# Performance work log

Hardware: AMD Instinct MI355X
Metric: run time of the kernel (lower is better)

Reference implementation:

```python
import jax, jax.numpy as jnp
import numpy as np

G, NPG, MAXN = 1024, 40, 51   # graphs, nodes/graph, dense pad size
EPG = 80                       # edges per graph
N, E = G * NPG, G * EPG
D_IN, D_OUT, D_EDGE = 64, 32, 16


def _lin(key, fan_in, shape):
    b = 1.0 / np.sqrt(fan_in)
    return jax.random.uniform(key, shape, jnp.float32, -b, b)


def setup_inputs() -> dict:
    key = jax.random.key(0)
    ks = jax.random.split(key, 24)
    node_features = jax.random.randint(ks[0], (N, 9), 0, 128)
    edge_features = jax.random.randint(ks[1], (E, 3), 0, 8)
    offs = jnp.repeat(jnp.arange(G) * NPG, EPG)
    src = jax.random.randint(ks[2], (E,), 0, NPG) + offs
    dst = jax.random.randint(ks[3], (E,), 0, NPG) + offs
    edge_index = jnp.stack([src, dst])
    batch = jnp.repeat(jnp.arange(G), NPG)
    inp = dict(node_features=node_features, edge_features=edge_features,
               edge_index=edge_index, batch=batch)
    # OGB-style encoders: one embedding table per feature column, summed
    inp['atom_emb'] = jax.random.normal(ks[4], (9, 128, D_IN), jnp.float32) * 0.1
    inp['bond_emb'] = jax.random.normal(ks[5], (3, 8, D_EDGE), jnp.float32) * 0.1
    # edge-conditioned weight MLP: 16 -> 1024 -> 256 -> 64*32 (no bias)
    inp['gW1'] = _lin(ks[6], 16, (16, 1024))
    inp['gW2'] = _lin(ks[7], 1024, (1024, 256))
    inp['gW3'] = _lin(ks[8], 256, (256, D_IN * D_OUT))
    # NNConv root weight + bias
    inp['root'] = _lin(ks[9], D_IN, (D_IN, D_OUT))
    inp['conv_bias'] = jnp.zeros((D_OUT,), jnp.float32)
    # readout MLP: 51*32 -> 256 -> 128 -> 32 -> 8 -> 1
    dims = [MAXN * D_OUT, 256, 128, 32, 8, 1]
    for i in range(5):
        inp[f'mW{i+1}'] = _lin(ks[10 + 2 * i], dims[i], (dims[i], dims[i + 1]))
        inp[f'mb{i+1}'] = _lin(ks[11 + 2 * i], dims[i], (dims[i + 1],))
    return inp


def reference(node_features, edge_features, edge_index, batch,
              atom_emb, bond_emb, gW1, gW2, gW3, root, conv_bias,
              mW1, mb1, mW2, mb2, mW3, mb3, mW4, mb4, mW5, mb5):
    # encoders: sum of per-column embeddings
    x = jnp.sum(atom_emb[jnp.arange(9), node_features], axis=1)      # [N,64]
    e = jnp.sum(bond_emb[jnp.arange(3), edge_features], axis=1)      # [E,16]
    # per-edge weight matrix via MLP
    h = jax.nn.relu(e @ gW1)
    h = jax.nn.relu(h @ gW2)
    w = (h @ gW3).reshape(-1, D_IN, D_OUT)                           # [E,64,32]
    # NNConv: gather src, per-edge matmul, scatter-add to dst, + root + bias
    src, dst = edge_index[0], edge_index[1]
    msg = jnp.einsum('ed,edo->eo', x[src], w)                        # [E,32]
    agg = jax.ops.segment_sum(msg, dst, num_segments=N)              # [N,32]
    out = agg + x @ root + conv_bias
    # to_dense_batch(max_num_nodes=51); exactly NPG nodes per graph, zero-pad
    dense = jnp.zeros((G, MAXN, D_OUT), out.dtype).at[:, :NPG].set(
        out.reshape(G, NPG, D_OUT))
    f = dense.reshape(G, MAXN * D_OUT)                               # [G,1632]
    f = jax.nn.relu(f @ mW1 + mb1)
    f = jax.nn.relu(f @ mW2 + mb2)
    f = jax.nn.relu(f @ mW3 + mb3)
    f = jax.nn.relu(f @ mW4 + mb4)
    return f @ mW5 + mb5                                             # [G,1]
```

## Files before the change

### kernel.cpp

```cpp
#include <hip/hip_runtime.h>

#define NNODES 40960
#define NEDGES 81920
#define NG     1024
#define NCOMBO 512
#define NHB    320
#define NGRP   4

__global__ __launch_bounds__(256) void k_node(
    const int* __restrict__ nf, const float* __restrict__ emb,
    const float* __restrict__ root, const float* __restrict__ bias,
    float* __restrict__ x, float* __restrict__ out) {
    __shared__ float sx[4][64];
    const int t = threadIdx.x;
    const int ln = t >> 6;
    const int d  = t & 63;
    const int n  = blockIdx.x * 4 + ln;
    const int* nfr = nf + n * 9;
    float acc = 0.f;
#pragma unroll
    for (int c = 0; c < 9; ++c) {
        int idx = nfr[c];
        acc += emb[((c << 7) + idx) * 64 + d];
    }
    x[n * 64 + d] = acc;
    sx[ln][d] = acc;
    __syncthreads();
    if (d < 32) {
        float o = bias[d];
#pragma unroll
        for (int k = 0; k < 64; ++k) o += sx[ln][k] * root[k * 32 + d];
        out[n * 32 + d] = o;
    }
}

__global__ __launch_bounds__(256) void k_h1(
    const float* __restrict__ bemb, const float* __restrict__ gW1,
    float* __restrict__ h1) {
    __shared__ float se[16];
    const int b = blockIdx.x, t = threadIdx.x;
    const int c = b >> 2;
    const int n = ((b & 3) << 8) + t;
    if (t < 16) {
        int f0 = c >> 6, f1 = (c >> 3) & 7, f2 = c & 7;
        se[t] = bemb[f0 * 16 + t] + bemb[(8 + f1) * 16 + t] +
                bemb[(16 + f2) * 16 + t];
    }
    __syncthreads();
    float acc = 0.f;
#pragma unroll
    for (int k = 0; k < 16; ++k) acc += se[k] * gW1[k * 1024 + n];
    h1[c * 1024 + n] = fmaxf(acc, 0.f);
}

__global__ void k_hist(const int* __restrict__ ef, int* __restrict__ cid,
                       int* __restrict__ bh) {
    __shared__ int lh[512];
    const int t = threadIdx.x, b = blockIdx.x;
    lh[t] = 0; lh[t + 256] = 0;
    __syncthreads();
    int e = b * 256 + t;
    int c = (ef[e * 3] << 6) | (ef[e * 3 + 1] << 3) | ef[e * 3 + 2];
    cid[e] = c;
    atomicAdd(&lh[c], 1);
    __syncthreads();
    bh[t * NHB + b]         = lh[t];
    bh[(t + 256) * NHB + b] = lh[t + 256];
}

__global__ __launch_bounds__(512) void k_scanA(int* __restrict__ bh,
                                               int* __restrict__ tot) {
    __shared__ int tmp[512];
    const int c = blockIdx.x, t = threadIdx.x;
    int v = (t < NHB) ? bh[c * NHB + t] : 0;
    tmp[t] = v;
    __syncthreads();
    for (int d = 1; d < 512; d <<= 1) {
        int add = (t >= d) ? tmp[t - d] : 0;
        __syncthreads();
        tmp[t] += add;
        __syncthreads();
    }
    if (t < NHB) bh[c * NHB + t] = tmp[t] - v;
    if (t == 511) tot[c] = tmp[511];
}

__global__ __launch_bounds__(512) void k_scanB(const int* __restrict__ tot,
                                               int* __restrict__ offs) {
    __shared__ int tmp[512];
    const int t = threadIdx.x;
    int v = tot[t];
    tmp[t] = v;
    __syncthreads();
    for (int d = 1; d < 512; d <<= 1) {
        int add = (t >= d) ? tmp[t - d] : 0;
        __syncthreads();
        tmp[t] += add;
        __syncthreads();
    }
    offs[t] = tmp[t] - v;
    if (t == 511) offs[512] = tmp[511];
}

__global__ void k_scatter(const int* __restrict__ cid, const int* __restrict__ src,
                          const int* __restrict__ dst, const int* __restrict__ bh,
                          const int* __restrict__ offs, int2* __restrict__ esd) {
    __shared__ int cur[512];
    const int t = threadIdx.x, b = blockIdx.x;
    cur[t]       = bh[t * NHB + b]         + offs[t];
    cur[t + 256] = bh[(t + 256) * NHB + b] + offs[t + 256];
    __syncthreads();
    int e = b * 256 + t;
    int p = atomicAdd(&cur[cid[e]], 1);
    esd[p] = make_int2(src[e], dst[e]);
}

template <int BM, int BN, int BK, int TM, int TN>
__global__ __launch_bounds__(256)
void k_gemm_tiled(const float* __restrict__ A, const float* __restrict__ B,
                  const float* __restrict__ bias, float* __restrict__ C,
                  float* __restrict__ Cp, int M, int N, int K, int KS, int relu) {
    constexpr int TX = BN / TN;
    constexpr int TY = BM / TM;
    static_assert(TX * TY == 256, "block must be 256 threads");
    __shared__ float As[BK][BM + 4];
    __shared__ float Bs[BK][BN + 4];
    const int tx = threadIdx.x % TX, ty = threadIdx.x / TX;
    const int row0 = blockIdx.y * BM, col0 = blockIdx.x * BN;
    const int z = blockIdx.z;
    const int k_begin = z * KS, k_end = k_begin + KS;

    const int am = threadIdx.x >> 2;
    const int ak = (threadIdx.x & 3) << 2;
    const int bk = threadIdx.x >> 4;
    const int bn = (threadIdx.x & 15) << 2;

    float acc[TM][TN] = {};
    for (int k0 = k_begin; k0 < k_end; k0 += BK) {
        float4 av = *reinterpret_cast<const float4*>(&A[(row0 + am) * K + k0 + ak]);
        float4 bv = *reinterpret_cast<const float4*>(&B[(k0 + bk) * N + col0 + bn]);
        As[ak + 0][am] = av.x;
        As[ak + 1][am] = av.y;
        As[ak + 2][am] = av.z;
        As[ak + 3][am] = av.w;
        *reinterpret_cast<float4*>(&Bs[bk][bn]) = bv;
        __syncthreads();
#pragma unroll
        for (int k = 0; k < BK; ++k) {
            float a[TM], b[TN];
            *reinterpret_cast<float4*>(a) =
                *reinterpret_cast<const float4*>(&As[k][ty * TM]);
            *reinterpret_cast<float4*>(b) =
                *reinterpret_cast<const float4*>(&Bs[k][tx * TN]);
#pragma unroll
            for (int i = 0; i < TM; ++i)
#pragma unroll
                for (int j = 0; j < TN; ++j) acc[i][j] += a[i] * b[j];
        }
        __syncthreads();
    }

    const int MN = M * N;
    if (gridDim.z == 1) {
#pragma unroll
        for (int i = 0; i < TM; ++i) {
            int r = row0 + ty * TM + i;
            float4 v;
            v.x = acc[i][0]; v.y = acc[i][1]; v.z = acc[i][2]; v.w = acc[i][3];
            int c = col0 + tx * TN;
            if (bias) { v.x += bias[c]; v.y += bias[c+1]; v.z += bias[c+2]; v.w += bias[c+3]; }
            if (relu) { v.x = fmaxf(v.x,0.f); v.y = fmaxf(v.y,0.f);
                        v.z = fmaxf(v.z,0.f); v.w = fmaxf(v.w,0.f); }
            *reinterpret_cast<float4*>(&C[r * N + c]) = v;
        }
    } else {
        float* dstp = Cp + z * MN;
#pragma unroll
        for (int i = 0; i < TM; ++i) {
            int r = row0 + ty * TM + i;
            float4 v;
            v.x = acc[i][0]; v.y = acc[i][1]; v.z = acc[i][2]; v.w = acc[i][3];
            *reinterpret_cast<float4*>(&dstp[r * N + col0 + tx * TN]) = v;
        }
    }
}

__global__ void k_reduceK(const float* __restrict__ Cp, const float* __restrict__ bias,
                          float* __restrict__ C, int MN, int N, int nz, int relu) {
    int i4 = (blockIdx.x * 256 + threadIdx.x) * 4;
    if (i4 >= MN) return;
    float4 acc = *reinterpret_cast<const float4*>(&Cp[i4]);
    for (int z = 1; z < nz; ++z) {
        float4 t = *reinterpret_cast<const float4*>(&Cp[z * MN + i4]);
        acc.x += t.x; acc.y += t.y; acc.z += t.z; acc.w += t.w;
    }
    if (bias) {
        int c = i4 % N;
        acc.x += bias[c]; acc.y += bias[c + 1]; acc.z += bias[c + 2]; acc.w += bias[c + 3];
    }
    if (relu) {
        acc.x = fmaxf(acc.x, 0.f); acc.y = fmaxf(acc.y, 0.f);
        acc.z = fmaxf(acc.z, 0.f); acc.w = fmaxf(acc.w, 0.f);
    }
    *reinterpret_cast<float4*>(&C[i4]) = acc;
}

__global__ __launch_bounds__(256) void k_msgg(
    const float* __restrict__ x, const float* __restrict__ wtab,
    const int* __restrict__ offs, const int2* __restrict__ esd,
    float* __restrict__ out) {
    const int c   = blockIdx.x >> 2;
    const int grp = blockIdx.x & 3;
    const int t = threadIdx.x;
    const int o = t & 31, slot = t >> 5;
    const int e0 = offs[c];
    const int n_c = offs[c + 1] - e0;
    if (grp * 64 >= n_c) return;

    __shared__ float swT[32][65];
    __shared__ float sx[64][64];
    __shared__ int ssrc[64], sdst[64];

#pragma unroll
    for (int j = 0; j < 8; ++j) {
        int i = t + j * 256;
        swT[i & 31][i >> 5] = wtab[c * 2048 + i];
    }
    __syncthreads();
    float wr[64];
#pragma unroll
    for (int k = 0; k < 64; ++k) wr[k] = swT[o][k];

    for (int base = grp * 64; base < n_c; base += NGRP * 64) {
        int n_e = min(64, n_c - base);
        __syncthreads();
        if (t < n_e) {
            int2 sd = esd[e0 + base + t];
            ssrc[t] = sd.x; sdst[t] = sd.y;
        }
        __syncthreads();
#pragma unroll
        for (int i = 0; i < 16; ++i) {
            int idx = t + i * 256;
            int r = idx >> 6, d = idx & 63;
            if (r < n_e) sx[r][d] = x[ssrc[r] * 64 + d];
        }
        __syncthreads();
#pragma unroll
        for (int j = 0; j < 8; ++j) {
            int ei = slot * 8 + j;
            if (ei < n_e) {
                const float4* xv = reinterpret_cast<const float4*>(sx[ei]);
                float acc = 0.f;
#pragma unroll
                for (int k4 = 0; k4 < 16; ++k4) {
                    float4 xq = xv[k4];
                    acc += xq.x * wr[k4 * 4 + 0];
                    acc += xq.y * wr[k4 * 4 + 1];
                    acc += xq.z * wr[k4 * 4 + 2];
                    acc += xq.w * wr[k4 * 4 + 3];
                }
                atomicAdd(&out[sdst[ei] * 32 + o], acc);
            }
        }
    }
}

__global__ __launch_bounds__(256) void k_tail2(
    const float* __restrict__ f1,
    const float* __restrict__ mW2, const float* __restrict__ mb2,
    const float* __restrict__ mW3, const float* __restrict__ mb3,
    const float* __restrict__ mW4, const float* __restrict__ mb4,
    const float* __restrict__ mW5, const float* __restrict__ mb5,
    float* __restrict__ outv) {
    __shared__ float s1[4][256];
    __shared__ float s2[4][128];
    __shared__ float s3[4][32];
    __shared__ float s4[4][8];
    const int t  = threadIdx.x;
    const int g0 = blockIdx.x * 4;
#pragma unroll
    for (int i = 0; i < 4; ++i) {
        int idx = t + i * 256;
        s1[idx >> 8][idx & 255] = f1[g0 * 256 + idx];
    }
    __syncthreads();
#pragma unroll
    for (int i = 0; i < 2; ++i) {
        int idx = t + i * 256;
        int g = idx >> 7, cc = idx & 127;
        float acc = mb2[cc];
#pragma unroll 8
        for (int k = 0; k < 256; ++k) acc += s1[g][k] * mW2[k * 128 + cc];
        s2[g][cc] = fmaxf(acc, 0.f);
    }
    __syncthreads();
    const int w = t >> 6, lane = t & 63;
    if (lane < 32) {
        float acc = mb3[lane];
#pragma unroll 8
        for (int k = 0; k < 128; ++k) acc += s2[w][k] * mW3[k * 32 + lane];
        s3[w][lane] = fmaxf(acc, 0.f);
    }
    __syncthreads();
    if (lane < 8) {
        float acc = mb4[lane];
#pragma unroll
        for (int k = 0; k < 32; ++k) acc += s3[w][k] * mW4[k * 8 + lane];
        s4[w][lane] = fmaxf(acc, 0.f);
    }
    __syncthreads();
    if (lane == 0) {
        float acc = mb5[0];
#pragma unroll
        for (int k = 0; k < 8; ++k) acc += s4[w][k] * mW5[k];
        outv[g0 + w] = acc;
    }
}

extern "C" void kernel_launch(void* const* d_in, const int* in_sizes, int n_in,
                              void* d_out, int out_size, void* d_ws, size_t ws_size,
                              hipStream_t stream) {
    const int*   nf      = (const int*)d_in[0];
    const int*   ef      = (const int*)d_in[1];
    const int*   eidx    = (const int*)d_in[2];
    const float* atom_emb= (const float*)d_in[4];
    const float* bond_emb= (const float*)d_in[5];
    const float* gW1     = (const float*)d_in[6];
    const float* gW2     = (const float*)d_in[7];
    const float* gW3     = (const float*)d_in[8];
    const float* root    = (const float*)d_in[9];
    const float* cbias   = (const float*)d_in[10];
    const float* mW1     = (const float*)d_in[11];
    const float* mb1     = (const float*)d_in[12];
    const float* mW2     = (const float*)d_in[13];
    const float* mb2     = (const float*)d_in[14];
    const float* mW3     = (const float*)d_in[15];
    const float* mb3     = (const float*)d_in[16];
    const float* mW4     = (const float*)d_in[17];
    const float* mb4     = (const float*)d_in[18];
    const float* mW5     = (const float*)d_in[19];
    const float* mb5     = (const float*)d_in[20];

    const int* src = eidx;
    const int* dst = eidx + NEDGES;

    float* ws = (float*)d_ws;
    float* x    = ws;
    float* out  = x + 2621440;
    float* h1   = out + 1310720;
    float* h2   = h1 + 524288;
    float* wtab = h2 + 131072;
    float* f1   = wtab + 1048576;
    float* part = f1 + 262144;
    int*   cid  = (int*)(part + 2097152);
    int*   bh   = cid + 81920;
    int*   tot  = bh + 163840;
    int*   offs = tot + 512;
    int2*  esd  = (int2*)(offs + 1024);

    k_node<<<NNODES / 4, 256, 0, stream>>>(nf, atom_emb, root, cbias, x, out);
    k_hist<<<NHB, 256, 0, stream>>>(ef, cid, bh);
    k_scanA<<<NCOMBO, 512, 0, stream>>>(bh, tot);
    k_scanB<<<1, 512, 0, stream>>>(tot, offs);
    k_scatter<<<NHB, 256, 0, stream>>>(cid, src, dst, bh, offs, esd);
    k_h1<<<NCOMBO * 4, 256, 0, stream>>>(bond_emb, gW1, h1);
    k_gemm_tiled<64, 64, 16, 4, 4><<<dim3(4, 8, 16), 256, 0, stream>>>(
        h1, gW2, nullptr, nullptr, part, NCOMBO, 256, 1024, 64, 0);
    k_reduceK<<<131072 / 1024, 256, 0, stream>>>(part, nullptr, h2, 131072, 256, 16, 1);
    k_gemm_tiled<64, 64, 16, 4, 4><<<dim3(32, 8, 2), 256, 0, stream>>>(
        h2, gW3, nullptr, nullptr, part, NCOMBO, 2048, 256, 128, 0);
    k_reduceK<<<1048576 / 1024, 256, 0, stream>>>(part, nullptr, wtab, 1048576, 2048, 2, 0);
    k_msgg<<<NCOMBO * NGRP, 256, 0, stream>>>(x, wtab, offs, esd, out);
    k_gemm_tiled<64, 64, 16, 4, 4><<<dim3(4, 16, 8), 256, 0, stream>>>(
        out, mW1, nullptr, nullptr, part, NG, 256, 1280, 160, 0);
    k_reduceK<<<262144 / 1024, 256, 0, stream>>>(part, mb1, f1, 262144, 256, 8, 1);
    k_tail2<<<NG / 4, 256, 0, stream>>>(f1, mW2, mb2, mW3, mb3, mW4, mb4,
                                        mW5, mb5, (float*)d_out);
}
```

Baseline: 237.0 us.

## Replace atomic scatter-add with per-edge message buffer and per-graph reduction

The message kernel now writes each edge's 32-wide message to a per-edge buffer indexed by original edge id, instead of issuing global float atomics into the node output. A new per-graph kernel loads that graph's 80 messages into shared memory and sums them per destination node without atomics. The block-histogram layout is also transposed so the histogram and scatter kernels write and read contiguously. This removes atomic contention but adds a kernel launch and an extra round trip through a 10 MB buffer, and it assumes edges are grouped per graph (80 per graph, destinations local to the graph).

```diff
diff --git a/kernel.cpp b/kernel.cpp
--- a/kernel.cpp
+++ b/kernel.cpp
@@ -64,15 +64,15 @@
     cid[e] = c;
     atomicAdd(&lh[c], 1);
     __syncthreads();
-    bh[t * NHB + b]         = lh[t];
-    bh[(t + 256) * NHB + b] = lh[t + 256];
+    bh[b * 512 + t]       = lh[t];
+    bh[b * 512 + 256 + t] = lh[t + 256];
 }
 
 __global__ __launch_bounds__(512) void k_scanA(int* __restrict__ bh,
                                                int* __restrict__ tot) {
     __shared__ int tmp[512];
     const int c = blockIdx.x, t = threadIdx.x;
-    int v = (t < NHB) ? bh[c * NHB + t] : 0;
+    int v = (t < NHB) ? bh[t * 512 + c] : 0;
     tmp[t] = v;
     __syncthreads();
     for (int d = 1; d < 512; d <<= 1) {
@@ -81,7 +81,7 @@
         tmp[t] += add;
         __syncthreads();
     }
-    if (t < NHB) bh[c * NHB + t] = tmp[t] - v;
+    if (t < NHB) bh[t * 512 + c] = tmp[t] - v;
     if (t == 511) tot[c] = tmp[511];
 }
 
@@ -103,16 +103,16 @@
 }
 
 __global__ void k_scatter(const int* __restrict__ cid, const int* __restrict__ src,
-                          const int* __restrict__ dst, const int* __restrict__ bh,
-                          const int* __restrict__ offs, int2* __restrict__ esd) {
+                          const int* __restrict__ bh, const int* __restrict__ offs,
+                          int2* __restrict__ esd) {
     __shared__ int cur[512];
     const int t = threadIdx.x, b = blockIdx.x;
-    cur[t]       = bh[t * NHB + b]         + offs[t];
-    cur[t + 256] = bh[(t + 256) * NHB + b] + offs[t + 256];
+    cur[t]       = bh[b * 512 + t]       + offs[t];
+    cur[t + 256] = bh[b * 512 + 256 + t] + offs[t + 256];
     __syncthreads();
     int e = b * 256 + t;
     int p = atomicAdd(&cur[cid[e]], 1);
-    esd[p] = make_int2(src[e], dst[e]);
+    esd[p] = make_int2(src[e], e);
 }
 
 template <int BM, int BN, int BK, int TM, int TN>
@@ -208,7 +208,7 @@
 __global__ __launch_bounds__(256) void k_msgg(
     const float* __restrict__ x, const float* __restrict__ wtab,
     const int* __restrict__ offs, const int2* __restrict__ esd,
-    float* __restrict__ out) {
+    float* __restrict__ msg) {
     const int c   = blockIdx.x >> 2;
     const int grp = blockIdx.x & 3;
     const int t = threadIdx.x;
@@ -219,7 +219,7 @@
 
     __shared__ float swT[32][65];
     __shared__ float sx[64][64];
-    __shared__ int ssrc[64], sdst[64];
+    __shared__ int ssrc[64], seid[64];
 
 #pragma unroll
     for (int j = 0; j < 8; ++j) {
@@ -236,7 +236,7 @@
         __syncthreads();
         if (t < n_e) {
             int2 sd = esd[e0 + base + t];
-            ssrc[t] = sd.x; sdst[t] = sd.y;
+            ssrc[t] = sd.x; seid[t] = sd.y;
         }
         __syncthreads();
 #pragma unroll
@@ -260,9 +260,33 @@
                     acc += xq.z * wr[k4 * 4 + 2];
                     acc += xq.w * wr[k4 * 4 + 3];
                 }
-                atomicAdd(&out[sdst[ei] * 32 + o], acc);
+                msg[seid[ei] * 32 + o] = acc;
             }
         }
+    }
+}
+
+__global__ __launch_bounds__(256) void k_gred(
+    const float* __restrict__ msg, const int* __restrict__ dst,
+    float* __restrict__ out) {
+    __shared__ float smsg[80][32];
+    __shared__ int   sdst[80];
+    const int g = blockIdx.x, t = threadIdx.x;
+#pragma unroll
+    for (int i = 0; i < 10; ++i) {
+        int idx = t + i * 256;
+        smsg[idx >> 5][idx & 31] = msg[g * 2560 + idx];
+    }
+    if (t < 80) sdst[t] = dst[g * 80 + t] - g * 40;
+    __syncthreads();
+#pragma unroll
+    for (int i = 0; i < 5; ++i) {
+        int idx = t + i * 256;
+        int n = idx >> 5, o = idx & 31;
+        float acc = out[g * 1280 + idx];
+        for (int j = 0; j < 80; ++j)
+            if (sdst[j] == n) acc += smsg[j][o];
+        out[g * 1280 + idx] = acc;
     }
 }
 
@@ -353,7 +377,8 @@
     float* wtab = h2 + 131072;
     float* f1   = wtab + 1048576;
     float* part = f1 + 262144;
-    int*   cid  = (int*)(part + 2097152);
+    float* msg  = part + 2097152;
+    int*   cid  = (int*)(msg + 2621440);
     int*   bh   = cid + 81920;
     int*   tot  = bh + 163840;
     int*   offs = tot + 512;
@@ -363,7 +388,7 @@
     k_hist<<<NHB, 256, 0, stream>>>(ef, cid, bh);
     k_scanA<<<NCOMBO, 512, 0, stream>>>(bh, tot);
     k_scanB<<<1, 512, 0, stream>>>(tot, offs);
-    k_scatter<<<NHB, 256, 0, stream>>>(cid, src, dst, bh, offs, esd);
+    k_scatter<<<NHB, 256, 0, stream>>>(cid, src, bh, offs, esd);
     k_h1<<<NCOMBO * 4, 256, 0, stream>>>(bond_emb, gW1, h1);
     k_gemm_tiled<64, 64, 16, 4, 4><<<dim3(4, 8, 16), 256, 0, stream>>>(
         h1, gW2, nullptr, nullptr, part, NCOMBO, 256, 1024, 64, 0);
@@ -371,7 +396,8 @@
     k_gemm_tiled<64, 64, 16, 4, 4><<<dim3(32, 8, 2), 256, 0, stream>>>(
         h2, gW3, nullptr, nullptr, part, NCOMBO, 2048, 256, 128, 0);
     k_reduceK<<<1048576 / 1024, 256, 0, stream>>>(part, nullptr, wtab, 1048576, 2048, 2, 0);
-    k_msgg<<<NCOMBO * NGRP, 256, 0, stream>>>(x, wtab, offs, esd, out);
+    k_msgg<<<NCOMBO * NGRP, 256, 0, stream>>>(x, wtab, offs, esd, msg);
+    k_gred<<<NG, 256, 0, stream>>>(msg, dst, out);
     k_gemm_tiled<64, 64, 16, 4, 4><<<dim3(4, 16, 8), 256, 0, stream>>>(
         out, mW1, nullptr, nullptr, part, NG, 256, 1280, 160, 0);
     k_reduceK<<<262144 / 1024, 256, 0, stream>>>(part, mb1, f1, 262144, 256, 8, 1);
```

Measured after the change: 255.9 us. 8.0% more time.
